# Kernel optimization log

Measured on AMD Instinct MI355X. Metric: run time of the kernel, lower is better.

## Reference

```python
import jax, jax.numpy as jnp
import numpy as np

EMBED_DIM = 1024
NUM_HEADS = 16
HEAD_DIM = EMBED_DIM // NUM_HEADS


def setup_inputs() -> dict:
    key = jax.random.key(0)
    k1, k2, k3, k4 = jax.random.split(key, 4)
    S, B = 2048, 2
    x = jax.random.normal(k1, (S, B, EMBED_DIM), dtype=jnp.float32)
    # xavier_uniform for in_proj_weight [3E, E]
    limit_in = float(np.sqrt(6.0 / (3 * EMBED_DIM + EMBED_DIM)))
    in_proj_weight = jax.random.uniform(k2, (3 * EMBED_DIM, EMBED_DIM), minval=-limit_in, maxval=limit_in, dtype=jnp.float32)
    in_proj_bias = jnp.zeros((3 * EMBED_DIM,), dtype=jnp.float32)
    # out_proj: nn.Linear default init (kaiming-uniform-ish); use uniform of similar scale
    limit_out = float(np.sqrt(1.0 / EMBED_DIM))
    out_proj_weight = jax.random.uniform(k3, (EMBED_DIM, EMBED_DIM), minval=-limit_out, maxval=limit_out, dtype=jnp.float32)
    out_proj_bias = jnp.zeros((EMBED_DIM,), dtype=jnp.float32)
    return {
        "x": x,
        "in_proj_weight": in_proj_weight,
        "in_proj_bias": in_proj_bias,
        "out_proj_weight": out_proj_weight,
        "out_proj_bias": out_proj_bias,
    }


def reference(x, in_proj_weight, in_proj_bias, out_proj_weight, out_proj_bias):
    S, B, E = x.shape
    H, D = NUM_HEADS, HEAD_DIM
    scaling = float(D) ** -0.5
    # fused QKV projection: [S, B, 3E]
    qkv = jnp.einsum("sbe,fe->sbf", x, in_proj_weight) + in_proj_bias
    q, k, v = jnp.split(qkv, 3, axis=-1)
    q = q * scaling
    # [S, B, E] -> [B*H, S, D]
    def to_heads(t):
        return t.reshape(S, B * H, D).transpose(1, 0, 2)
    q, k, v = to_heads(q), to_heads(k), to_heads(v)
    # attention scores [B*H, S, S]
    scores = jnp.einsum("btd,bsd->bts", q, k)
    weights = jax.nn.softmax(scores, axis=-1)
    # dropout p=0.0 -> identity
    attn = jnp.einsum("bts,bsd->btd", weights, v)  # [B*H, S, D]
    attn = attn.transpose(1, 0, 2).reshape(S, B, E)
    out = jnp.einsum("sbe,fe->sbf", attn, out_proj_weight) + out_proj_bias
    return out
```

## Files before the change

kernel.cpp:

```cpp
#include <hip/hip_runtime.h>

typedef __bf16 bf16_t;
typedef __attribute__((ext_vector_type(8))) __bf16 bf16x8;
typedef __attribute__((ext_vector_type(4))) __bf16 bf16x4;
typedef __attribute__((ext_vector_type(4))) float f32x4;
typedef __attribute__((ext_vector_type(16))) float f32x16;
typedef __attribute__((ext_vector_type(2))) unsigned uint2v;

#define MFMA16(a, b, c) __builtin_amdgcn_mfma_f32_16x16x32_bf16((a), (b), (c), 0, 0, 0)
#define MFMA32(a, b, c) __builtin_amdgcn_mfma_f32_32x32x16_bf16((a), (b), (c), 0, 0, 0)
#define LOG2E 1.44269504088896f

__device__ __forceinline__ void async16(const bf16_t* g, bf16_t* l) {
    __builtin_amdgcn_global_load_lds(
        (const __attribute__((address_space(1))) unsigned int*)g,
        (__attribute__((address_space(3))) unsigned int*)l, 16, 0, 0);
}

__device__ __forceinline__ unsigned pack2(float a, float b) {
    union { bf16_t e[2]; unsigned u; } x;
    x.e[0] = (bf16_t)a; x.e[1] = (bf16_t)b;
    return x.u;
}

__device__ __forceinline__ void pl32swap(unsigned& a, unsigned& b) {
    uint2v r = __builtin_amdgcn_permlane32_swap(a, b, false, false);
    a = r[0]; b = r[1];
}

__global__ __launch_bounds__(256) void conv3(
    const float* __restrict__ s0, const float* __restrict__ s1,
    const float* __restrict__ s2, bf16_t* __restrict__ dst,
    int n0, int n1)
{
    const int i = (blockIdx.x * 256 + threadIdx.x) * 8;
    const float* src;
    int off;
    if (i < n0)           { src = s0; off = 0; }
    else if (i < n0 + n1) { src = s1; off = n0; }
    else                  { src = s2; off = n0 + n1; }
    const float4 a = *reinterpret_cast<const float4*>(src + i - off);
    const float4 b = *reinterpret_cast<const float4*>(src + i - off + 4);
    bf16x8 o;
    o[0] = (bf16_t)a.x; o[1] = (bf16_t)a.y; o[2] = (bf16_t)a.z; o[3] = (bf16_t)a.w;
    o[4] = (bf16_t)b.x; o[5] = (bf16_t)b.y; o[6] = (bf16_t)b.z; o[7] = (bf16_t)b.w;
    *reinterpret_cast<bf16x8*>(dst + i) = o;
}

template <int MT, bool F32OUT, bool VST>
__global__ __launch_bounds__(256, 3) void gemm_nt_lds(
    const bf16_t* __restrict__ W, const bf16_t* __restrict__ X,
    const float* __restrict__ bias, void* __restrict__ Cv,
    bf16_t* __restrict__ vtp,
    int N, int K, int scale_lim, float qscale, int fpx)
{
    constexpr int NJ = MT / 32;
    __shared__ bf16_t As[2][128 * 32];
    __shared__ bf16_t Bs[2][MT * 32];

    const int lane = threadIdx.x & 63;
    const int wv   = threadIdx.x >> 6;
    const int l15  = lane & 15;
    const int qd   = lane >> 4;

    const int id = blockIdx.x;
    const int x8 = id & 7, k = id >> 3;
    const int fb = ((k % fpx) * 8 + x8) * 128;
    const int mb = (k / fpx) * MT;
    const int fw = (wv & 1) * 64;
    const int mw = (wv >> 1) * (MT / 2);

    f32x4 acc[4][NJ] = {};

    auto stage = [&](int set, int k0) {
#pragma unroll
        for (int t = 0; t < 2; t++) {
            const int p = (wv * 2 + t) * 64 + lane;
            const int r = p >> 2, cl = (p & 3) ^ (r & 3);
            async16(W + (size_t)(fb + r) * K + k0 + cl * 8,
                    &As[set][(wv * 2 + t) * 512]);
        }
#pragma unroll
        for (int t = 0; t < MT / 64; t++) {
            const int p = (wv * (MT / 64) + t) * 64 + lane;
            const int r = p >> 2, cl = (p & 3) ^ (r & 3);
            async16(X + (size_t)(mb + r) * K + k0 + cl * 8,
                    &Bs[set][(wv * (MT / 64) + t) * 512]);
        }
    };

    stage(0, 0);
    int set = 0;
    for (int k0 = 0; k0 < K; k0 += 32) {
        __syncthreads();
        if (k0 + 32 < K) stage(set ^ 1, k0 + 32);

        const int s3 = l15 & 3;
        bf16x8 a[4], bb[NJ];
#pragma unroll
        for (int i = 0; i < 4; i++)
            a[i] = *reinterpret_cast<const bf16x8*>(
                &As[set][(fw + i * 16 + l15) * 32 + ((qd ^ s3) * 8)]);
#pragma unroll
        for (int j = 0; j < NJ; j++)
            bb[j] = *reinterpret_cast<const bf16x8*>(
                &Bs[set][(mw + j * 16 + l15) * 32 + ((qd ^ s3) * 8)]);
#pragma unroll
        for (int i = 0; i < 4; i++)
#pragma unroll
            for (int j = 0; j < NJ; j++)
                acc[i][j] = MFMA16(a[i], bb[j], acc[i][j]);
        set ^= 1;
    }

    const float scale = (fb < scale_lim) ? qscale : 1.0f;
    const bool vblk = VST && (fb >= 2048);
#pragma unroll
    for (int i = 0; i < 4; i++) {
        const int f0 = fb + fw + i * 16 + qd * 4;
        float bs[4];
#pragma unroll
        for (int r = 0; r < 4; r++) bs[r] = bias[f0 + r];
#pragma unroll
        for (int j = 0; j < NJ; j++) {
            const int m = mb + mw + j * 16 + l15;
            if (F32OUT) {
                float4 o;
                o.x = (acc[i][j][0] + bs[0]) * scale;
                o.y = (acc[i][j][1] + bs[1]) * scale;
                o.z = (acc[i][j][2] + bs[2]) * scale;
                o.w = (acc[i][j][3] + bs[3]) * scale;
                *reinterpret_cast<float4*>((float*)Cv + (size_t)m * N + f0) = o;
            } else if (vblk) {
                const int s  = m >> 1;
                const int b2 = (m & 1) << 4;
#pragma unroll
                for (int r = 0; r < 4; r++) {
                    const int fv = f0 + r - 2048;
                    vtp[(size_t)((b2 + (fv >> 6)) * 64 + (fv & 63)) * 2048 + s] =
                        (bf16_t)(acc[i][j][r] + bs[r]);
                }
            } else {
                bf16x4 o;
#pragma unroll
                for (int r = 0; r < 4; r++)
                    o[r] = (bf16_t)((acc[i][j][r] + bs[r]) * scale);
                *reinterpret_cast<bf16x4*>((bf16_t*)Cv + (size_t)m * N + f0) = o;
            }
        }
    }
}

__global__ __launch_bounds__(256, 2) void flash_attn(
    const bf16_t* __restrict__ qkv, const bf16_t* __restrict__ vT,
    bf16_t* __restrict__ attn, int S, int B)
{
    const int E3 = 3072, E = 1024;
    const int bh = blockIdx.x, b = bh >> 4, h = bh & 15;
    const int tid = threadIdx.x, lane = tid & 63, wv = tid >> 6;
    const int qw = wv & 1;
    const int pr = wv >> 1;
    const int l31 = lane & 31, half = lane >> 5;

    __shared__ bf16_t Kt[2][2][64 * 64];
    __shared__ bf16_t Vt[2][2][64 * 64];
    __shared__ float  lsh[2][64];

    const int q0 = blockIdx.y * 128 + qw * 64;

    bf16x8 qf[2][4];
#pragma unroll
    for (int qt = 0; qt < 2; qt++) {
        const bf16_t* qp = qkv + (size_t)((q0 + qt * 32 + l31) * B + b) * E3 + h * 64;
#pragma unroll
        for (int ks = 0; ks < 4; ks++)
            qf[qt][ks] = *reinterpret_cast<const bf16x8*>(qp + ks * 16 + half * 8);
    }

    f32x16 oacc[2][2] = {};
    float lrun[2] = {0.0f, 0.0f};

    auto stage = [&](int set, int kv) {
#pragma unroll
        for (int t = 0; t < 4; t++) {
            const int p = (qw * 4 + t) * 64 + lane;
            const int r = p >> 3, cl = (p & 7) ^ (r & 7);
            async16(qkv + (size_t)((kv + r) * B + b) * E3 + E + h * 64 + cl * 8,
                    &Kt[pr][set][(qw * 4 + t) * 512]);
            async16(vT + (size_t)(bh * 64 + r) * 2048 + kv + cl * 8,
                    &Vt[pr][set][(qw * 4 + t) * 512]);
        }
    };

    const int kvbase = pr * (S / 2);
    const int NIT = S / 128;

    stage(0, kvbase);
    int set = 0;
    for (int it = 0; it < NIT; it++) {
        __syncthreads();
        if (it + 1 < NIT) stage(set ^ 1, kvbase + (it + 1) * 64);

        const bf16_t* K_ = Kt[pr][set];
        const bf16_t* V_ = Vt[pr][set];

        union PF { unsigned u[4]; bf16x8 v; };
        PF pf[2][4];
#pragma unroll
        for (int nt = 0; nt < 2; nt++) {
            const int r = nt * 32 + l31;
            const int r7 = r & 7;
            bf16x8 kf[4];
#pragma unroll
            for (int ks = 0; ks < 4; ks++)
                kf[ks] = *reinterpret_cast<const bf16x8*>(
                    K_ + r * 64 + (((ks * 2 + half) ^ r7) * 8));
#pragma unroll
            for (int qt = 0; qt < 2; qt++) {
                f32x16 st = {};
                __builtin_amdgcn_s_setprio(1);
#pragma unroll
                for (int ks = 0; ks < 4; ks++)
                    st = MFMA32(kf[ks], qf[qt][ks], st);
                __builtin_amdgcn_s_setprio(0);
                float ls = 0.0f;
                unsigned q8[8];
#pragma unroll
                for (int g = 0; g < 4; g++) {
                    const float p0 = __builtin_amdgcn_exp2f(st[4 * g]);
                    const float p1 = __builtin_amdgcn_exp2f(st[4 * g + 1]);
                    const float p2 = __builtin_amdgcn_exp2f(st[4 * g + 2]);
                    const float p3 = __builtin_amdgcn_exp2f(st[4 * g + 3]);
                    ls += (p0 + p1) + (p2 + p3);
                    q8[2 * g]     = pack2(p0, p1);
                    q8[2 * g + 1] = pack2(p2, p3);
                }
                lrun[qt] += ls;
                pl32swap(q8[0], q8[2]); pl32swap(q8[1], q8[3]);
                pl32swap(q8[4], q8[6]); pl32swap(q8[5], q8[7]);
                pf[qt][nt * 2 + 0].u[0] = q8[0]; pf[qt][nt * 2 + 0].u[1] = q8[1];
                pf[qt][nt * 2 + 0].u[2] = q8[2]; pf[qt][nt * 2 + 0].u[3] = q8[3];
                pf[qt][nt * 2 + 1].u[0] = q8[4]; pf[qt][nt * 2 + 1].u[1] = q8[5];
                pf[qt][nt * 2 + 1].u[2] = q8[6]; pf[qt][nt * 2 + 1].u[3] = q8[7];
            }
        }
        __builtin_amdgcn_s_setprio(1);
#pragma unroll
        for (int kn = 0; kn < 4; kn++)
#pragma unroll
            for (int dt = 0; dt < 2; dt++) {
                const int d = dt * 32 + l31;
                bf16x8 vf = *reinterpret_cast<const bf16x8*>(
                    V_ + d * 64 + (((kn * 2 + half) ^ (d & 7)) * 8));
                oacc[0][dt] = MFMA32(vf, pf[0][kn].v, oacc[0][dt]);
                oacc[1][dt] = MFMA32(vf, pf[1][kn].v, oacc[1][dt]);
            }
        __builtin_amdgcn_s_setprio(0);
        set ^= 1;
    }

    __syncthreads();
    float lr[2];
#pragma unroll
    for (int qt = 0; qt < 2; qt++) lr[qt] = lrun[qt] + __shfl_xor(lrun[qt], 32);

    float* fo = reinterpret_cast<float*>(&Kt[0][0][0]) + qw * 4096;

    if (pr == 1) {
#pragma unroll
        for (int qt = 0; qt < 2; qt++) {
            const int ql = qt * 32 + l31;
            lsh[qw][ql] = lr[qt];
#pragma unroll
            for (int dt = 0; dt < 2; dt++)
#pragma unroll
                for (int g = 0; g < 4; g++)
#pragma unroll
                    for (int r = 0; r < 4; r++) {
                        const int d = dt * 32 + g * 8 + half * 4 + r;
                        fo[d * 64 + ql] = oacc[qt][dt][4 * g + r];
                    }
        }
    }
    __syncthreads();
    if (pr == 0) {
#pragma unroll
        for (int qt = 0; qt < 2; qt++) {
            const int ql = qt * 32 + l31;
            const float inv = 1.0f / (lr[qt] + lsh[qw][ql]);
            const int qrow = q0 + qt * 32 + l31;
#pragma unroll
            for (int dt = 0; dt < 2; dt++)
#pragma unroll
                for (int g = 0; g < 4; g++) {
                    bf16x4 o;
#pragma unroll
                    for (int r = 0; r < 4; r++) {
                        const int d = dt * 32 + g * 8 + half * 4 + r;
                        o[r] = (bf16_t)((oacc[qt][dt][4 * g + r] + fo[d * 64 + ql]) * inv);
                    }
                    *reinterpret_cast<bf16x4*>(attn + (size_t)(qrow * B + b) * E +
                                               h * 64 + dt * 32 + g * 8 + half * 4) = o;
                }
        }
    }
}

extern "C" void kernel_launch(void* const* d_in, const int* in_sizes, int n_in,
                              void* d_out, int out_size, void* d_ws, size_t ws_size,
                              hipStream_t stream) {
    const float* x  = (const float*)d_in[0];
    const float* wi = (const float*)d_in[1];
    const float* bi = (const float*)d_in[2];
    const float* wo = (const float*)d_in[3];
    const float* bo = (const float*)d_in[4];
    float* out = (float*)d_out;

    const int S = 2048, B = 2, E = 1024;
    const int M = S * B;

    bf16_t* xb   = (bf16_t*)d_ws;
    bf16_t* wib  = xb  + (size_t)M * E;
    bf16_t* wob  = wib + (size_t)3 * E * E;
    bf16_t* qkv  = wob + (size_t)E * E;
    bf16_t* vT   = qkv + (size_t)M * 3 * E;
    bf16_t* attn = xb;

    const int n0 = M * E, n1 = 3 * E * E, n2 = E * E;
    conv3<<<(n0 + n1 + n2) / 8 / 256, 256, 0, stream>>>(x, wi, wo, xb, n0, n1);

    gemm_nt_lds<128, false, true><<<(3 * E / 128) * (M / 128), 256, 0, stream>>>(
        wib, xb, bi, qkv, vT, 3 * E, E, E, 0.125f * LOG2E, (3 * E / 128) / 8);

    flash_attn<<<dim3(B * 16, S / 128), 256, 0, stream>>>(qkv, vT, attn, S, B);

    gemm_nt_lds<64, true, false><<<(E / 128) * (M / 64), 256, 0, stream>>>(
        wob, attn, bo, out, nullptr, E, E, 0, 1.0f, (E / 128) / 8);
}
```

Baseline: 188.7 us.

## Replace QKV projection GEMM with 256x256-tile 8-wave kernel using phased MFMA scheduling

```diff
diff --git a/kernel.cpp b/kernel.cpp
--- a/kernel.cpp
+++ b/kernel.cpp
@@ -26,6 +26,12 @@
 __device__ __forceinline__ void pl32swap(unsigned& a, unsigned& b) {
     uint2v r = __builtin_amdgcn_permlane32_swap(a, b, false, false);
     a = r[0]; b = r[1];
+}
+
+__device__ __forceinline__ void pbar() {
+    asm volatile("" ::: "memory");
+    __builtin_amdgcn_s_barrier();
+    asm volatile("" ::: "memory");
 }
 
 __global__ __launch_bounds__(256) void conv3(
@@ -47,12 +53,172 @@
     *reinterpret_cast<bf16x8*>(dst + i) = o;
 }
 
-template <int MT, bool F32OUT, bool VST>
+__global__ __launch_bounds__(512, 2) void gemm_qkv(
+    const bf16_t* __restrict__ W, const bf16_t* __restrict__ X,
+    const float* __restrict__ bias, bf16_t* __restrict__ qkv,
+    bf16_t* __restrict__ vtp)
+{
+    constexpr int K = 1024;
+    constexpr int NSTEP = K / 64;
+
+    __shared__ bf16_t lds[2][32768];
+
+    const int tid  = threadIdx.x;
+    const int lane = tid & 63;
+    const int wv   = tid >> 6;
+    const int wm   = wv >> 2;
+    const int wn   = wv & 3;
+    const int l15  = lane & 15;
+    const int qd   = lane >> 4;
+
+    const int id = blockIdx.x;
+    const int x8 = id & 7, k = id >> 3;
+    const int mb = ((k & 1) * 8 + x8) * 256;
+    const int fb = (k >> 1) * 256;
+
+    f32x4 acc[8][4] = {};
+
+    auto stage = [&](int set, int k0) {
+        bf16_t* Ab = lds[set];
+        bf16_t* Bb = lds[set] + 16384;
+#pragma unroll
+        for (int h = 0; h < 2; h++) {
+#pragma unroll
+            for (int t = 0; t < 2; t++) {
+                const int p = (wv * 2 + t) * 64 + lane;
+                const int r = p >> 3;
+                const int c = (p & 7) ^ (r & 7);
+                async16(W + (size_t)(fb + h * 128 + r) * K + k0 + c * 8,
+                        Ab + h * 8192 + (wv * 2 + t) * 512);
+                async16(X + (size_t)(mb + h * 128 + r) * K + k0 + c * 8,
+                        Bb + h * 8192 + (wv * 2 + t) * 512);
+            }
+        }
+    };
+
+    stage(0, 0);
+    for (int s = 0; s < NSTEP; s++) {
+        const int set = s & 1;
+        __syncthreads();
+        if (s + 1 < NSTEP) stage(set ^ 1, (s + 1) * 64);
+
+        const bf16_t* Ab = lds[set];
+        const bf16_t* Bb = lds[set] + 16384;
+
+        bf16x8 a0[4][2], a1[4][2], b0[2][2], b1[2][2];
+
+#pragma unroll
+        for (int i = 0; i < 4; i++) {
+            const int r = wm * 128 + i * 16 + l15;
+            a0[i][0] = *reinterpret_cast<const bf16x8*>(
+                Ab + r * 64 + ((qd ^ (r & 7)) * 8));
+            a0[i][1] = *reinterpret_cast<const bf16x8*>(
+                Ab + r * 64 + (((4 + qd) ^ (r & 7)) * 8));
+        }
+#pragma unroll
+        for (int j = 0; j < 2; j++) {
+            const int r = wn * 64 + j * 16 + l15;
+            b0[j][0] = *reinterpret_cast<const bf16x8*>(
+                Bb + r * 64 + ((qd ^ (r & 7)) * 8));
+            b0[j][1] = *reinterpret_cast<const bf16x8*>(
+                Bb + r * 64 + (((4 + qd) ^ (r & 7)) * 8));
+        }
+        __builtin_amdgcn_s_setprio(1);
+#pragma unroll
+        for (int i = 0; i < 4; i++)
+#pragma unroll
+            for (int j = 0; j < 2; j++) {
+                acc[i][j] = MFMA16(a0[i][0], b0[j][0], acc[i][j]);
+                acc[i][j] = MFMA16(a0[i][1], b0[j][1], acc[i][j]);
+            }
+        __builtin_amdgcn_s_setprio(0);
+        pbar();
+
+#pragma unroll
+        for (int i = 0; i < 4; i++) {
+            const int r = wm * 128 + (i + 4) * 16 + l15;
+            a1[i][0] = *reinterpret_cast<const bf16x8*>(
+                Ab + r * 64 + ((qd ^ (r & 7)) * 8));
+            a1[i][1] = *reinterpret_cast<const bf16x8*>(
+                Ab + r * 64 + (((4 + qd) ^ (r & 7)) * 8));
+        }
+        __builtin_amdgcn_s_setprio(1);
+#pragma unroll
+        for (int i = 0; i < 4; i++)
+#pragma unroll
+            for (int j = 0; j < 2; j++) {
+                acc[i + 4][j] = MFMA16(a1[i][0], b0[j][0], acc[i + 4][j]);
+                acc[i + 4][j] = MFMA16(a1[i][1], b0[j][1], acc[i + 4][j]);
+            }
+        __builtin_amdgcn_s_setprio(0);
+        pbar();
+
+#pragma unroll
+        for (int j = 0; j < 2; j++) {
+            const int r = wn * 64 + (j + 2) * 16 + l15;
+            b1[j][0] = *reinterpret_cast<const bf16x8*>(
+                Bb + r * 64 + ((qd ^ (r & 7)) * 8));
+            b1[j][1] = *reinterpret_cast<const bf16x8*>(
+                Bb + r * 64 + (((4 + qd) ^ (r & 7)) * 8));
+        }
+        __builtin_amdgcn_s_setprio(1);
+#pragma unroll
+        for (int i = 0; i < 4; i++)
+#pragma unroll
+            for (int j = 0; j < 2; j++) {
+                acc[i + 4][j + 2] = MFMA16(a1[i][0], b1[j][0], acc[i + 4][j + 2]);
+                acc[i + 4][j + 2] = MFMA16(a1[i][1], b1[j][1], acc[i + 4][j + 2]);
+            }
+        __builtin_amdgcn_s_setprio(0);
+        pbar();
+
+        __builtin_amdgcn_s_setprio(1);
+#pragma unroll
+        for (int i = 0; i < 4; i++)
+#pragma unroll
+            for (int j = 0; j < 2; j++) {
+                acc[i][j + 2] = MFMA16(a0[i][0], b1[j][0], acc[i][j + 2]);
+                acc[i][j + 2] = MFMA16(a0[i][1], b1[j][1], acc[i][j + 2]);
+            }
+        __builtin_amdgcn_s_setprio(0);
+    }
+
+    const float scale = (fb < 1024) ? 0.125f * LOG2E : 1.0f;
+    const bool vblk = (fb >= 2048);
+#pragma unroll
+    for (int i = 0; i < 8; i++) {
+        const int f0 = fb + wm * 128 + i * 16 + qd * 4;
+        float bs[4];
+#pragma unroll
+        for (int r = 0; r < 4; r++) bs[r] = bias[f0 + r];
+#pragma unroll
+        for (int j = 0; j < 4; j++) {
+            const int m = mb + wn * 64 + j * 16 + l15;
+            if (vblk) {
+                const int sIdx = m >> 1;
+                const int b2   = (m & 1) << 4;
+#pragma unroll
+                for (int r = 0; r < 4; r++) {
+                    const int fv = f0 + r - 2048;
+                    vtp[(size_t)((b2 + (fv >> 6)) * 64 + (fv & 63)) * 2048 + sIdx] =
+                        (bf16_t)(acc[i][j][r] + bs[r]);
+                }
+            } else {
+                bf16x4 o;
+#pragma unroll
+                for (int r = 0; r < 4; r++)
+                    o[r] = (bf16_t)((acc[i][j][r] + bs[r]) * scale);
+                *reinterpret_cast<bf16x4*>(qkv + (size_t)m * 3072 + f0) = o;
+            }
+        }
+    }
+}
+
+template <int MT, bool F32OUT>
 __global__ __launch_bounds__(256, 3) void gemm_nt_lds(
     const bf16_t* __restrict__ W, const bf16_t* __restrict__ X,
     const float* __restrict__ bias, void* __restrict__ Cv,
-    bf16_t* __restrict__ vtp,
-    int N, int K, int scale_lim, float qscale, int fpx)
+    int N, int K, int fpx)
 {
     constexpr int NJ = MT / 32;
     __shared__ bf16_t As[2][128 * 32];
@@ -113,8 +279,6 @@
         set ^= 1;
     }
 
-    const float scale = (fb < scale_lim) ? qscale : 1.0f;
-    const bool vblk = VST && (fb >= 2048);
 #pragma unroll
     for (int i = 0; i < 4; i++) {
         const int f0 = fb + fw + i * 16 + qd * 4;
@@ -126,25 +290,16 @@
             const int m = mb + mw + j * 16 + l15;
             if (F32OUT) {
                 float4 o;
-                o.x = (acc[i][j][0] + bs[0]) * scale;
-                o.y = (acc[i][j][1] + bs[1]) * scale;
-                o.z = (acc[i][j][2] + bs[2]) * scale;
-                o.w = (acc[i][j][3] + bs[3]) * scale;
+                o.x = acc[i][j][0] + bs[0];
+                o.y = acc[i][j][1] + bs[1];
+                o.z = acc[i][j][2] + bs[2];
+                o.w = acc[i][j][3] + bs[3];
                 *reinterpret_cast<float4*>((float*)Cv + (size_t)m * N + f0) = o;
-            } else if (vblk) {
-                const int s  = m >> 1;
-                const int b2 = (m & 1) << 4;
-#pragma unroll
-                for (int r = 0; r < 4; r++) {
-                    const int fv = f0 + r - 2048;
-                    vtp[(size_t)((b2 + (fv >> 6)) * 64 + (fv & 63)) * 2048 + s] =
-                        (bf16_t)(acc[i][j][r] + bs[r]);
-                }
             } else {
                 bf16x4 o;
 #pragma unroll
                 for (int r = 0; r < 4; r++)
-                    o[r] = (bf16_t)((acc[i][j][r] + bs[r]) * scale);
+                    o[r] = (bf16_t)(acc[i][j][r] + bs[r]);
                 *reinterpret_cast<bf16x4*>((bf16_t*)Cv + (size_t)m * N + f0) = o;
             }
         }
@@ -329,11 +484,10 @@
     const int n0 = M * E, n1 = 3 * E * E, n2 = E * E;
     conv3<<<(n0 + n1 + n2) / 8 / 256, 256, 0, stream>>>(x, wi, wo, xb, n0, n1);
 
-    gemm_nt_lds<128, false, true><<<(3 * E / 128) * (M / 128), 256, 0, stream>>>(
-        wib, xb, bi, qkv, vT, 3 * E, E, E, 0.125f * LOG2E, (3 * E / 128) / 8);
+    gemm_qkv<<<192, 512, 0, stream>>>(wib, xb, bi, qkv, vT);
 
     flash_attn<<<dim3(B * 16, S / 128), 256, 0, stream>>>(qkv, vT, attn, S, B);
 
-    gemm_nt_lds<64, true, false><<<(E / 128) * (M / 64), 256, 0, stream>>>(
-        wob, attn, bo, out, nullptr, E, E, 0, 1.0f, (E / 128) / 8);
-}
+    gemm_nt_lds<64, true><<<(E / 128) * (M / 64), 256, 0, stream>>>(
+        wob, attn, bo, out, E, E, 1);
+}
```

New measurement: 190.0 us. About the same (+0.7%).
